# Kernel tuning notes

Measured on AMD Instinct MI355X. Metric: run time of the kernel, lower is better.

Reference implementation:

```python
import jax, jax.numpy as jnp
import numpy as np

B, V = 128, 128000

def setup_inputs() -> dict:
    key = jax.random.key(0)
    k1, k2, k3 = jax.random.split(key, 3)
    logits = jax.random.normal(k1, (B, V), dtype=jnp.float32)
    # mix of greedy (temp==0) and sampling rows, as the torch module handles both
    u = jax.random.uniform(k2, (B,), dtype=jnp.float32, minval=0.1, maxval=1.5)
    temperatures = jnp.where(jnp.arange(B) % 4 == 0, 0.0, u)
    # Exponential(1) samples standing in for torch's empty_like().exponential_(1)
    exp_noise = jax.random.exponential(k3, (B, V), dtype=jnp.float32)
    return {"logits": logits, "temperatures": temperatures, "exp_noise": exp_noise}

def reference(logits, temperatures, exp_noise):
    temps = temperatures.reshape(-1)                      # [B]
    scaled = logits.astype(jnp.float32)                   # [B, V]
    greedy = temps == 0.0                                 # [B]
    safe_t = jnp.where(greedy, 1.0, temps)[:, None]       # avoid div-by-zero; masked out below
    # E = Exp(1).clamp_min(1e-10).log(); scaled_sample = logits/T - E (Gumbel-max)
    e_log = jnp.log(jnp.maximum(exp_noise, 1e-10))        # [B, V]
    sampled = scaled / safe_t - e_log                     # [B, V]
    scaled = jnp.where(greedy[:, None], scaled, sampled)  # predicated, no dynamic shapes
    return jnp.argmax(scaled, axis=-1)                    # [B] int
```

## Files before the change

kernel.cpp:

```cpp
#include <hip/hip_runtime.h>
#include <cstdint>
#include <math.h>

#define BB 128
#define VV 128000
#define SPLITS 8
#define CHUNK (VV / SPLITS)
#define TPB 256

__device__ __forceinline__ void combine(float& bv, int& bi, float v, int i) {
    if (v > bv || (v == bv && i < bi)) { bv = v; bi = i; }
}

__global__ __launch_bounds__(TPB) void sampler_partial(
    const float* __restrict__ logits,
    const float* __restrict__ temps,
    const float* __restrict__ noise,
    float* __restrict__ pmax,
    int*   __restrict__ pidx)
{
    const int blk = blockIdx.x;
    const int row = blk / SPLITS;
    const int seg = blk % SPLITS;

    const float t = temps[row];
    const bool greedy = (t == 0.0f);
    const float invt = greedy ? 1.0f : (1.0f / t);

    const float* lrow = logits + (size_t)row * VV;
    const float* nrow = noise  + (size_t)row * VV;

    const int start = seg * CHUNK;
    const int end   = start + CHUNK;

    float bv = -INFINITY;
    int   bi = 0x7fffffff;

    if (greedy) {
        for (int i = start + (int)threadIdx.x * 4; i < end; i += TPB * 4) {
            float4 l = *reinterpret_cast<const float4*>(lrow + i);
            combine(bv, bi, l.x, i + 0);
            combine(bv, bi, l.y, i + 1);
            combine(bv, bi, l.z, i + 2);
            combine(bv, bi, l.w, i + 3);
        }
    } else {
        for (int i = start + (int)threadIdx.x * 4; i < end; i += TPB * 4) {
            float4 l = *reinterpret_cast<const float4*>(lrow + i);
            float4 e = *reinterpret_cast<const float4*>(nrow + i);
            float s0 = l.x * invt - logf(fmaxf(e.x, 1e-10f));
            float s1 = l.y * invt - logf(fmaxf(e.y, 1e-10f));
            float s2 = l.z * invt - logf(fmaxf(e.z, 1e-10f));
            float s3 = l.w * invt - logf(fmaxf(e.w, 1e-10f));
            combine(bv, bi, s0, i + 0);
            combine(bv, bi, s1, i + 1);
            combine(bv, bi, s2, i + 2);
            combine(bv, bi, s3, i + 3);
        }
    }

    #pragma unroll
    for (int off = 32; off > 0; off >>= 1) {
        float ov = __shfl_down(bv, off, 64);
        int   oi = __shfl_down(bi, off, 64);
        combine(bv, bi, ov, oi);
    }

    __shared__ float sv[TPB / 64];
    __shared__ int   si[TPB / 64];
    const int lane = threadIdx.x & 63;
    const int wave = threadIdx.x >> 6;
    if (lane == 0) { sv[wave] = bv; si[wave] = bi; }
    __syncthreads();
    if (threadIdx.x == 0) {
        #pragma unroll
        for (int w = 1; w < TPB / 64; ++w) combine(bv, bi, sv[w], si[w]);
        pmax[blk] = bv;
        pidx[blk] = bi;
    }
}

__global__ __launch_bounds__(128) void sampler_reduce(
    const float* __restrict__ pmax,
    const int*   __restrict__ pidx,
    int* __restrict__ out)
{
    const int r = blockIdx.x * blockDim.x + threadIdx.x;
    if (r < BB) {
        float bv = -INFINITY;
        int   bi = 0x7fffffff;
        #pragma unroll
        for (int s = 0; s < SPLITS; ++s)
            combine(bv, bi, pmax[r * SPLITS + s], pidx[r * SPLITS + s]);
        out[r] = bi;
    }
}

extern "C" void kernel_launch(void* const* d_in, const int* in_sizes, int n_in,
                              void* d_out, int out_size, void* d_ws, size_t ws_size,
                              hipStream_t stream) {
    const float* logits = (const float*)d_in[0];
    const float* temps  = (const float*)d_in[1];
    const float* noise  = (const float*)d_in[2];
    int* out = (int*)d_out;

    float* pmax = (float*)d_ws;
    int*   pidx = (int*)((char*)d_ws + sizeof(float) * BB * SPLITS);

    sampler_partial<<<BB * SPLITS, TPB, 0, stream>>>(logits, temps, noise, pmax, pidx);
    sampler_reduce<<<1, 128, 0, stream>>>(pmax, pidx, out);
}
```

Measured before the change: 144.1 us.

## Split rows into 25 chunks, unroll all loads, pack argmax into 64-bit keys

Raises the per-row split from 8 to 25 so that each block handles exactly 5 float4 loads per thread. All loads are issued up front in a fully unrolled loop, which exposes more memory-level parallelism and produces 3200 blocks in place of 1024. The value/index pair is packed into a single sortable 64-bit key, so each reduction step needs one shuffle and one compare. This relies on CHUNK dividing exactly into TPB*4*ITERS and on tie-breaking toward the lowest index through the inverted index bits. NaN ordering may differ from the reference.

Measured after the change: 141.8 us. No clear change (-1.6%).

```diff
diff --git a/kernel.cpp b/kernel.cpp
--- a/kernel.cpp
+++ b/kernel.cpp
@@ -4,20 +4,25 @@
 
 #define BB 128
 #define VV 128000
-#define SPLITS 8
+#define SPLITS 25
 #define CHUNK (VV / SPLITS)
 #define TPB 256
+#define ITERS 5
 
-__device__ __forceinline__ void combine(float& bv, int& bi, float v, int i) {
-    if (v > bv || (v == bv && i < bi)) { bv = v; bi = i; }
+__device__ __forceinline__ uint32_t sortable(float f) {
+    uint32_t u = __float_as_uint(f);
+    return (u & 0x80000000u) ? ~u : (u | 0x80000000u);
+}
+
+__device__ __forceinline__ uint64_t kmax(uint64_t a, uint64_t b) {
+    return a > b ? a : b;
 }
 
 __global__ __launch_bounds__(TPB) void sampler_partial(
     const float* __restrict__ logits,
     const float* __restrict__ temps,
     const float* __restrict__ noise,
-    float* __restrict__ pmax,
-    int*   __restrict__ pidx)
+    uint64_t* __restrict__ pkey)
 {
     const int blk = blockIdx.x;
     const int row = blk / SPLITS;
@@ -27,73 +32,77 @@
     const bool greedy = (t == 0.0f);
     const float invt = greedy ? 1.0f : (1.0f / t);
 
-    const float* lrow = logits + (size_t)row * VV;
-    const float* nrow = noise  + (size_t)row * VV;
+    const float* lrow = logits + (size_t)row * VV + seg * CHUNK;
+    const float* nrow = noise  + (size_t)row * VV + seg * CHUNK;
 
-    const int start = seg * CHUNK;
-    const int end   = start + CHUNK;
+    const int base = (int)threadIdx.x * 4;
+
+    float4 l[ITERS];
+    #pragma unroll
+    for (int j = 0; j < ITERS; ++j)
+        l[j] = *reinterpret_cast<const float4*>(lrow + base + j * (TPB * 4));
 
     float bv = -INFINITY;
-    int   bi = 0x7fffffff;
+    int   bi = 0;
 
     if (greedy) {
-        for (int i = start + (int)threadIdx.x * 4; i < end; i += TPB * 4) {
-            float4 l = *reinterpret_cast<const float4*>(lrow + i);
-            combine(bv, bi, l.x, i + 0);
-            combine(bv, bi, l.y, i + 1);
-            combine(bv, bi, l.z, i + 2);
-            combine(bv, bi, l.w, i + 3);
+        #pragma unroll
+        for (int j = 0; j < ITERS; ++j) {
+            const int i0 = seg * CHUNK + base + j * (TPB * 4);
+            const float v[4] = { l[j].x, l[j].y, l[j].z, l[j].w };
+            #pragma unroll
+            for (int c = 0; c < 4; ++c) {
+                if (v[c] > bv) { bv = v[c]; bi = i0 + c; }
+            }
         }
     } else {
-        for (int i = start + (int)threadIdx.x * 4; i < end; i += TPB * 4) {
-            float4 l = *reinterpret_cast<const float4*>(lrow + i);
-            float4 e = *reinterpret_cast<const float4*>(nrow + i);
-            float s0 = l.x * invt - logf(fmaxf(e.x, 1e-10f));
-            float s1 = l.y * invt - logf(fmaxf(e.y, 1e-10f));
-            float s2 = l.z * invt - logf(fmaxf(e.z, 1e-10f));
-            float s3 = l.w * invt - logf(fmaxf(e.w, 1e-10f));
-            combine(bv, bi, s0, i + 0);
-            combine(bv, bi, s1, i + 1);
-            combine(bv, bi, s2, i + 2);
-            combine(bv, bi, s3, i + 3);
+        float4 e[ITERS];
+        #pragma unroll
+        for (int j = 0; j < ITERS; ++j)
+            e[j] = *reinterpret_cast<const float4*>(nrow + base + j * (TPB * 4));
+        #pragma unroll
+        for (int j = 0; j < ITERS; ++j) {
+            const int i0 = seg * CHUNK + base + j * (TPB * 4);
+            const float lv[4] = { l[j].x, l[j].y, l[j].z, l[j].w };
+            const float ev[4] = { e[j].x, e[j].y, e[j].z, e[j].w };
+            #pragma unroll
+            for (int c = 0; c < 4; ++c) {
+                const float s = lv[c] * invt - logf(fmaxf(ev[c], 1e-10f));
+                if (s > bv) { bv = s; bi = i0 + c; }
+            }
         }
     }
 
+    uint64_t key = ((uint64_t)sortable(bv) << 32) | (uint32_t)(~(uint32_t)bi);
+
     #pragma unroll
     for (int off = 32; off > 0; off >>= 1) {
-        float ov = __shfl_down(bv, off, 64);
-        int   oi = __shfl_down(bi, off, 64);
-        combine(bv, bi, ov, oi);
+        uint64_t ok = __shfl_down(key, off, 64);
+        key = kmax(key, ok);
     }
 
-    __shared__ float sv[TPB / 64];
-    __shared__ int   si[TPB / 64];
+    __shared__ uint64_t sk[TPB / 64];
     const int lane = threadIdx.x & 63;
     const int wave = threadIdx.x >> 6;
-    if (lane == 0) { sv[wave] = bv; si[wave] = bi; }
+    if (lane == 0) sk[wave] = key;
     __syncthreads();
     if (threadIdx.x == 0) {
         #pragma unroll
-        for (int w = 1; w < TPB / 64; ++w) combine(bv, bi, sv[w], si[w]);
-        pmax[blk] = bv;
-        pidx[blk] = bi;
+        for (int w = 1; w < TPB / 64; ++w) key = kmax(key, sk[w]);
+        pkey[blk] = key;
     }
 }
 
-__global__ __launch_bounds__(128) void sampler_reduce(
-    const float* __restrict__ pmax,
-    const int*   __restrict__ pidx,
+__global__ __launch_bounds__(BB) void sampler_reduce(
+    const uint64_t* __restrict__ pkey,
     int* __restrict__ out)
 {
-    const int r = blockIdx.x * blockDim.x + threadIdx.x;
-    if (r < BB) {
-        float bv = -INFINITY;
-        int   bi = 0x7fffffff;
-        #pragma unroll
-        for (int s = 0; s < SPLITS; ++s)
-            combine(bv, bi, pmax[r * SPLITS + s], pidx[r * SPLITS + s]);
-        out[r] = bi;
-    }
+    const int r = threadIdx.x;
+    uint64_t key = pkey[r * SPLITS];
+    #pragma unroll
+    for (int s = 1; s < SPLITS; ++s)
+        key = kmax(key, pkey[r * SPLITS + s]);
+    out[r] = (int)(~(uint32_t)(key & 0xffffffffu));
 }
 
 extern "C" void kernel_launch(void* const* d_in, const int* in_sizes, int n_in,
@@ -104,9 +113,8 @@
     const float* noise  = (const float*)d_in[2];
     int* out = (int*)d_out;
 
-    float* pmax = (float*)d_ws;
-    int*   pidx = (int*)((char*)d_ws + sizeof(float) * BB * SPLITS);
+    uint64_t* pkey = (uint64_t*)d_ws;
 
-    sampler_partial<<<BB * SPLITS, TPB, 0, stream>>>(logits, temps, noise, pmax, pidx);
-    sampler_reduce<<<1, 128, 0, stream>>>(pmax, pidx, out);
+    sampler_partial<<<BB * SPLITS, TPB, 0, stream>>>(logits, temps, noise, pkey);
+    sampler_reduce<<<1, BB, 0, stream>>>(pkey, out);
 }
```
